# Performance work log

Hardware: AMD Instinct MI355X
Metric: run time of the kernel (lower is better)

## Reference

```python
import jax, jax.numpy as jnp
import numpy as np

REGION_NUM = 8  # DRConv2d default region_num


def setup_inputs() -> dict:
    key = jax.random.key(0)
    ks = jax.random.split(key, 10)
    B, H, W = 4, 256, 256
    C = 64   # n_fea_middle
    r = REGION_NUM
    s = 0.05
    return {
        "rgb":  jax.random.normal(ks[0], (B, 3, H, W), jnp.float32),
        "edge": jax.random.normal(ks[1], (B, 1, H, W), jnp.float32),
        # conv1: 1x1, 4 -> C
        "W1":  jax.random.normal(ks[2], (C, 4), jnp.float32) * s,
        "b1":  jax.random.normal(ks[3], (C,), jnp.float32) * s,
        # DRConv kernel-generator stage 1: Conv2d(C, r*r, 1)
        "Wk1": jax.random.normal(ks[4], (r * r, C), jnp.float32) * s,
        "bk1": jax.random.normal(ks[5], (r * r,), jnp.float32) * s,
        # stage 2: Conv2d(r*r, r*C*C, 1, groups=r) -> per group: r inputs, C*C outputs
        "Wk2": jax.random.normal(ks[6], (r, C * C, r), jnp.float32) * s,
        "bk2": jax.random.normal(ks[7], (r, C * C), jnp.float32) * s,
        # conv_guide: Conv2d(C, r, 1)
        "Wg":  jax.random.normal(ks[8], (r, C), jnp.float32) * s,
        "bg":  jax.random.normal(ks[9], (r,), jnp.float32) * s,
    }


def reference(rgb, edge, W1, b1, Wk1, bk1, Wk2, bk2, Wg, bg):
    r = REGION_NUM
    B = rgb.shape[0]
    # concat rgb+edge, 1x1 conv to n_fea_middle
    x = jnp.concatenate([rgb, edge], axis=1)                       # B,4,H,W
    x1 = jnp.einsum('bihw,oi->bohw', x, W1) + b1[None, :, None, None]  # B,C,H,W
    C = x1.shape[1]
    # ---- DRConv2d(C, C, kernel_size=1, region_num=r) ----
    # kernel-generating branch: AdaptiveAvgPool2d(1) == global mean for k=1
    g = jnp.mean(x1, axis=(2, 3))                                  # B,C
    t = jax.nn.sigmoid(g @ Wk1.T + bk1)                            # B,r*r
    tg = t.reshape(B, r, r)                                        # grouped 1x1 conv, groups=r
    k = jnp.einsum('bgi,goi->bgo', tg, Wk2) + bk2[None]            # B,r,C*C
    kernel = k.reshape(B, r, C, C)                                 # B,r,Cout,Cin
    # cross-correlation: per-batch, per-region 1x1 conv of x1 with generated kernel
    region_out = jnp.einsum('bchw,broc->brohw', x1, kernel)        # B,r,Cout,H,W
    # guide branch + hard region routing (asign_index forward)
    guide = jnp.einsum('bchw,rc->brhw', x1, Wg) + bg[None, :, None, None]  # B,r,H,W
    mask = jax.nn.one_hot(jnp.argmax(guide, axis=1), r, axis=1, dtype=x1.dtype)  # B,r,H,W
    out = jnp.sum(region_out * mask[:, :, None], axis=1)           # B,Cout,H,W
    return out
```

## Files before the change

kernel.cpp:

```cpp
#include <hip/hip_runtime.h>


#define HW_ 65536

__device__ double g_part[128];
__device__ double g_WgP[32];
__device__ double g_bgP[8];
__device__ __align__(16) float g_Wm[8192];
__device__ __align__(16) float g_Bm[2048];

typedef float f4v __attribute__((ext_vector_type(4)));

__global__ void k_sum(const float* __restrict__ rgb, const float* __restrict__ edge) {
    int plane = blockIdx.x;
    int chunk = blockIdx.y;
    int b = plane >> 2, ch = plane & 3;
    const float* src = (ch < 3) ? rgb + (size_t)(b * 3 + ch) * HW_
                                : edge + (size_t)b * HW_;
    src += chunk * 8192;
    int t = threadIdx.x;
    double s = 0.0;
    #pragma unroll
    for (int p = 0; p < 8; ++p) {
        float4 v = *(const float4*)(src + (p * 256 + t) * 4);
        s += (double)v.x + (double)v.y + (double)v.z + (double)v.w;
    }
    #pragma unroll
    for (int off = 32; off; off >>= 1) s += __shfl_down(s, off);
    __shared__ double wsum[4];
    if ((t & 63) == 0) wsum[t >> 6] = s;
    __syncthreads();
    if (t == 0) g_part[plane * 8 + chunk] = wsum[0] + wsum[1] + wsum[2] + wsum[3];
}

__global__ void k_params(const float* __restrict__ W1, const float* __restrict__ b1,
                         const float* __restrict__ Wk1, const float* __restrict__ bk1,
                         const float* __restrict__ Wk2, const float* __restrict__ bk2,
                         const float* __restrict__ Wg, const float* __restrict__ bg) {
    int blk = blockIdx.x;
    int b = blk >> 3, gr = blk & 7;
    int t = threadIdx.x;
    __shared__ double xm[16];
    __shared__ double gsh[64];
    __shared__ double tt_sh[8];
    __shared__ double red[4][64][5];

    if (t < 16) {
        double s = 0;
        #pragma unroll
        for (int i = 0; i < 8; ++i) s += g_part[t * 8 + i];
        xm[t] = s * (1.0 / 65536.0);
    }
    __syncthreads();
    if (t < 64) {
        double acc = (double)b1[t];
        #pragma unroll
        for (int j = 0; j < 4; ++j) acc += (double)W1[t * 4 + j] * xm[b * 4 + j];
        gsh[t] = acc;
    }
    __syncthreads();
    if (t < 8) {
        int j = gr * 8 + t;
        double z = (double)bk1[j];
        for (int c = 0; c < 64; ++c) z += (double)Wk1[j * 64 + c] * gsh[c];
        tt_sh[t] = 1.0 / (1.0 + exp(-z));
    }
    if (blk == 0) {
        if (t >= 64 && t < 96) {
            int r = (t - 64) >> 2, j = (t - 64) & 3;
            double a = 0;
            for (int c = 0; c < 64; ++c)
                a += (double)Wg[r * 64 + c] * (double)W1[c * 4 + j];
            g_WgP[t - 64] = a;
        } else if (t >= 96 && t < 104) {
            int r = t - 96;
            double a = (double)bg[r];
            for (int c = 0; c < 64; ++c)
                a += (double)Wg[r * 64 + c] * (double)b1[c];
            g_bgP[r] = a;
        }
    }
    __syncthreads();

    int o = t & 63, cq = t >> 6;
    double tt[8];
    #pragma unroll
    for (int i = 0; i < 8; ++i) tt[i] = tt_sh[i];
    double aw0 = 0, aw1 = 0, aw2 = 0, aw3 = 0, ab = 0;
    const float* wk2p = Wk2 + ((size_t)gr * 4096 + o * 64) * 8;
    const float* bk2p = bk2 + (size_t)gr * 4096 + o * 64;
    for (int c = cq * 16; c < cq * 16 + 16; ++c) {
        double ker = (double)bk2p[c];
        #pragma unroll
        for (int i = 0; i < 8; ++i)
            ker += tt[i] * (double)wk2p[c * 8 + i];
        aw0 += ker * (double)W1[c * 4 + 0];
        aw1 += ker * (double)W1[c * 4 + 1];
        aw2 += ker * (double)W1[c * 4 + 2];
        ab  += ker * (double)b1[c];
        aw3 += ker * (double)W1[c * 4 + 3];
    }
    red[cq][o][0] = aw0; red[cq][o][1] = aw1; red[cq][o][2] = aw2;
    red[cq][o][3] = aw3; red[cq][o][4] = ab;
    __syncthreads();
    if (t < 64) {
        double w0 = 0, w1 = 0, w2 = 0, w3 = 0, bb = 0;
        #pragma unroll
        for (int q = 0; q < 4; ++q) {
            w0 += red[q][t][0]; w1 += red[q][t][1]; w2 += red[q][t][2];
            w3 += red[q][t][3]; bb += red[q][t][4];
        }
        float* w = g_Wm + ((size_t)blk * 64 + t) * 4;
        w[0] = (float)w0; w[1] = (float)w1; w[2] = (float)w2; w[3] = (float)w3;
        g_Bm[blk * 64 + t] = (float)bb;
    }
}

__launch_bounds__(256)
__global__ void k_main(const float* __restrict__ rgb, const float* __restrict__ edge,
                       float* __restrict__ out) {
    __shared__ __align__(16) float sW[8 * 68];
    __shared__ __align__(16) float sB[8 * 20];
    __shared__ double sWg[32];
    __shared__ double sBg[8];
    int t = threadIdx.x;
    int b = blockIdx.y;
    int z = blockIdx.z;

    {
        if (t < 128) {
            int r = t >> 4, ol = t & 15;
            const float4* src = (const float4*)g_Wm;
            *(float4*)&sW[r * 68 + ol * 4] = src[(size_t)(b * 8 + r) * 64 + z * 16 + ol];
        } else {
            int idx = t - 128;
            int r = idx >> 4, ol = idx & 15;
            sB[r * 20 + ol] = g_Bm[(size_t)(b * 8 + r) * 64 + z * 16 + ol];
        }
        if (t < 32) sWg[t] = g_WgP[t];
        else if (t < 40) sBg[t - 32] = g_bgP[t - 32];
    }
    __syncthreads();

    float wg[32], bgf[8];
    #pragma unroll
    for (int i = 0; i < 32; ++i) wg[i] = (float)sWg[i];
    #pragma unroll
    for (int r = 0; r < 8; ++r) bgf[r] = (float)sBg[r];

    int pxb = (blockIdx.x * 256 + t) * 4;
    float xa[4], xb[4], xc[4], xd[4];
    {
        float4 v0 = *(const float4*)(rgb  + (size_t)(b * 3 + 0) * HW_ + pxb);
        float4 v1 = *(const float4*)(rgb  + (size_t)(b * 3 + 1) * HW_ + pxb);
        float4 v2 = *(const float4*)(rgb  + (size_t)(b * 3 + 2) * HW_ + pxb);
        float4 v3 = *(const float4*)(edge + (size_t)b * HW_ + pxb);
        xa[0] = v0.x; xa[1] = v0.y; xa[2] = v0.z; xa[3] = v0.w;
        xb[0] = v1.x; xb[1] = v1.y; xb[2] = v1.z; xb[3] = v1.w;
        xc[0] = v2.x; xc[1] = v2.y; xc[2] = v2.z; xc[3] = v2.w;
        xd[0] = v3.x; xd[1] = v3.y; xd[2] = v3.z; xd[3] = v3.w;
    }

    int reg[4];
    #pragma unroll
    for (int p = 0; p < 4; ++p) {
        float m1 = -1e30f, m2 = -1e30f; int bi = 0;
        #pragma unroll
        for (int r = 0; r < 8; ++r) {
            float gv = bgf[r] + wg[r * 4 + 0] * xa[p] + wg[r * 4 + 1] * xb[p]
                              + wg[r * 4 + 2] * xc[p] + wg[r * 4 + 3] * xd[p];
            if (gv > m1) { m2 = m1; m1 = gv; bi = r; }
            else if (gv > m2) { m2 = gv; }
        }
        if (m1 - m2 < 1e-4f) {
            double da = xa[p], db = xb[p], dc = xc[p], dd = xd[p];
            double bm = -1e300; bi = 0;
            #pragma unroll
            for (int r = 0; r < 8; ++r) {
                double gv = sBg[r] + sWg[r * 4 + 0] * da + sWg[r * 4 + 1] * db
                                   + sWg[r * 4 + 2] * dc + sWg[r * 4 + 3] * dd;
                if (gv > bm) { bm = gv; bi = r; }
            }
        }
        reg[p] = bi;
    }

    int base[4], bbase[4];
    #pragma unroll
    for (int p = 0; p < 4; ++p) { base[p] = reg[p] * 68; bbase[p] = reg[p] * 20; }

    float* outp = out + (size_t)(b * 64 + z * 16) * HW_ + pxb;
    #pragma unroll
    for (int oq = 0; oq < 4; ++oq) {
        float res[4][4];
        #pragma unroll
        for (int p = 0; p < 4; ++p) {
            float4 bq = *(const float4*)&sB[bbase[p] + oq * 4];
            float bqa[4] = {bq.x, bq.y, bq.z, bq.w};
            #pragma unroll
            for (int k = 0; k < 4; ++k) {
                float4 w = *(const float4*)&sW[base[p] + (oq * 4 + k) * 4];
                res[k][p] = bqa[k] + w.x * xa[p] + w.y * xb[p]
                                   + w.z * xc[p] + w.w * xd[p];
            }
        }
        #pragma unroll
        for (int k = 0; k < 4; ++k) {
            f4v pk; pk.x = res[k][0]; pk.y = res[k][1];
            pk.z = res[k][2]; pk.w = res[k][3];
            __builtin_nontemporal_store(pk, (f4v*)(outp + (size_t)(oq * 4 + k) * HW_));
        }
    }
}

extern "C" void kernel_launch(void* const* d_in, const int* in_sizes, int n_in,
                              void* d_out, int out_size, void* d_ws, size_t ws_size,
                              hipStream_t stream) {
    (void)d_ws; (void)ws_size;
    const float* rgb  = (const float*)d_in[0];
    const float* edge = (const float*)d_in[1];
    const float* W1   = (const float*)d_in[2];
    const float* b1   = (const float*)d_in[3];
    const float* Wk1  = (const float*)d_in[4];
    const float* bk1  = (const float*)d_in[5];
    const float* Wk2  = (const float*)d_in[6];
    const float* bk2  = (const float*)d_in[7];
    const float* Wg   = (const float*)d_in[8];
    const float* bg   = (const float*)d_in[9];
    float* out = (float*)d_out;

    k_sum<<<dim3(16, 8), 256, 0, stream>>>(rgb, edge);
    k_params<<<32, 256, 0, stream>>>(W1, b1, Wk1, bk1, Wk2, bk2, Wg, bg);
    k_main<<<dim3(64, 4, 4), 256, 0, stream>>>(rgb, edge, out);
}
```

Measured before the change: 113.0 us.

## Double grid parallelism, warp-parallelize param dot products, hoist input loads

```diff
diff --git a/kernel.cpp b/kernel.cpp
--- a/kernel.cpp
+++ b/kernel.cpp
@@ -3,13 +3,16 @@
 
 #define HW_ 65536
 
-__device__ double g_part[128];
+__device__ double g_part[256];
 __device__ double g_WgP[32];
 __device__ double g_bgP[8];
+__device__ float  g_WgPf[32];
+__device__ float  g_bgPf[8];
 __device__ __align__(16) float g_Wm[8192];
 __device__ __align__(16) float g_Bm[2048];
 
 typedef float f4v __attribute__((ext_vector_type(4)));
+typedef float f2v __attribute__((ext_vector_type(2)));
 
 __global__ void k_sum(const float* __restrict__ rgb, const float* __restrict__ edge) {
     int plane = blockIdx.x;
@@ -17,12 +20,12 @@
     int b = plane >> 2, ch = plane & 3;
     const float* src = (ch < 3) ? rgb + (size_t)(b * 3 + ch) * HW_
                                 : edge + (size_t)b * HW_;
-    src += chunk * 8192;
+    src += chunk * 4096;
     int t = threadIdx.x;
     double s = 0.0;
     #pragma unroll
-    for (int p = 0; p < 8; ++p) {
-        float4 v = *(const float4*)(src + (p * 256 + t) * 4);
+    for (int p = 0; p < 4; ++p) {
+        float4 v = ((const float4*)src)[p * 256 + t];
         s += (double)v.x + (double)v.y + (double)v.z + (double)v.w;
     }
     #pragma unroll
@@ -30,7 +33,7 @@
     __shared__ double wsum[4];
     if ((t & 63) == 0) wsum[t >> 6] = s;
     __syncthreads();
-    if (t == 0) g_part[plane * 8 + chunk] = wsum[0] + wsum[1] + wsum[2] + wsum[3];
+    if (t == 0) g_part[plane * 16 + chunk] = wsum[0] + wsum[1] + wsum[2] + wsum[3];
 }
 
 __global__ void k_params(const float* __restrict__ W1, const float* __restrict__ b1,
@@ -40,6 +43,7 @@
     int blk = blockIdx.x;
     int b = blk >> 3, gr = blk & 7;
     int t = threadIdx.x;
+    int w = t >> 6, l = t & 63;
     __shared__ double xm[16];
     __shared__ double gsh[64];
     __shared__ double tt_sh[8];
@@ -48,7 +52,7 @@
     if (t < 16) {
         double s = 0;
         #pragma unroll
-        for (int i = 0; i < 8; ++i) s += g_part[t * 8 + i];
+        for (int i = 0; i < 16; ++i) s += g_part[t * 16 + i];
         xm[t] = s * (1.0 / 65536.0);
     }
     __syncthreads();
@@ -59,25 +63,29 @@
         gsh[t] = acc;
     }
     __syncthreads();
-    if (t < 8) {
-        int j = gr * 8 + t;
-        double z = (double)bk1[j];
-        for (int c = 0; c < 64; ++c) z += (double)Wk1[j * 64 + c] * gsh[c];
-        tt_sh[t] = 1.0 / (1.0 + exp(-z));
+    #pragma unroll
+    for (int q = 0; q < 2; ++q) {
+        int jj = w * 2 + q;
+        int j = gr * 8 + jj;
+        double prod = (double)Wk1[j * 64 + l] * gsh[l];
+        #pragma unroll
+        for (int off = 32; off; off >>= 1) prod += __shfl_down(prod, off);
+        if (l == 0) tt_sh[jj] = 1.0 / (1.0 + exp(-(prod + (double)bk1[j])));
     }
     if (blk == 0) {
-        if (t >= 64 && t < 96) {
-            int r = (t - 64) >> 2, j = (t - 64) & 3;
-            double a = 0;
-            for (int c = 0; c < 64; ++c)
-                a += (double)Wg[r * 64 + c] * (double)W1[c * 4 + j];
-            g_WgP[t - 64] = a;
-        } else if (t >= 96 && t < 104) {
-            int r = t - 96;
-            double a = (double)bg[r];
-            for (int c = 0; c < 64; ++c)
-                a += (double)Wg[r * 64 + c] * (double)b1[c];
-            g_bgP[r] = a;
+        for (int d = w; d < 40; d += 4) {
+            double prod;
+            if (d < 32) prod = (double)Wg[(d >> 2) * 64 + l] * (double)W1[l * 4 + (d & 3)];
+            else        prod = (double)Wg[(d - 32) * 64 + l] * (double)b1[l];
+            #pragma unroll
+            for (int off = 32; off; off >>= 1) prod += __shfl_down(prod, off);
+            if (l == 0) {
+                if (d < 32) { g_WgP[d] = prod; g_WgPf[d] = (float)prod; }
+                else {
+                    double a = (double)bg[d - 32] + prod;
+                    g_bgP[d - 32] = a; g_bgPf[d - 32] = (float)a;
+                }
+            }
         }
     }
     __syncthreads();
@@ -110,13 +118,13 @@
             w0 += red[q][t][0]; w1 += red[q][t][1]; w2 += red[q][t][2];
             w3 += red[q][t][3]; bb += red[q][t][4];
         }
-        float* w = g_Wm + ((size_t)blk * 64 + t) * 4;
-        w[0] = (float)w0; w[1] = (float)w1; w[2] = (float)w2; w[3] = (float)w3;
+        float* wv = g_Wm + ((size_t)blk * 64 + t) * 4;
+        wv[0] = (float)w0; wv[1] = (float)w1; wv[2] = (float)w2; wv[3] = (float)w3;
         g_Bm[blk * 64 + t] = (float)bb;
     }
 }
 
-__launch_bounds__(256)
+__launch_bounds__(256, 6)
 __global__ void k_main(const float* __restrict__ rgb, const float* __restrict__ edge,
                        float* __restrict__ out) {
     __shared__ __align__(16) float sW[8 * 68];
@@ -127,11 +135,17 @@
     int b = blockIdx.y;
     int z = blockIdx.z;
 
+    int pxb = (blockIdx.x * 256 + t) * 2;
+    f2v v0 = *(const f2v*)(rgb  + (size_t)(b * 3 + 0) * HW_ + pxb);
+    f2v v1 = *(const f2v*)(rgb  + (size_t)(b * 3 + 1) * HW_ + pxb);
+    f2v v2 = *(const f2v*)(rgb  + (size_t)(b * 3 + 2) * HW_ + pxb);
+    f2v v3 = *(const f2v*)(edge + (size_t)b * HW_ + pxb);
+
     {
         if (t < 128) {
             int r = t >> 4, ol = t & 15;
-            const float4* src = (const float4*)g_Wm;
-            *(float4*)&sW[r * 68 + ol * 4] = src[(size_t)(b * 8 + r) * 64 + z * 16 + ol];
+            *(float4*)&sW[r * 68 + ol * 4] =
+                ((const float4*)g_Wm)[(size_t)(b * 8 + r) * 64 + z * 16 + ol];
         } else {
             int idx = t - 128;
             int r = idx >> 4, ol = idx & 15;
@@ -144,26 +158,21 @@
 
     float wg[32], bgf[8];
     #pragma unroll
-    for (int i = 0; i < 32; ++i) wg[i] = (float)sWg[i];
-    #pragma unroll
-    for (int r = 0; r < 8; ++r) bgf[r] = (float)sBg[r];
-
-    int pxb = (blockIdx.x * 256 + t) * 4;
-    float xa[4], xb[4], xc[4], xd[4];
-    {
-        float4 v0 = *(const float4*)(rgb  + (size_t)(b * 3 + 0) * HW_ + pxb);
-        float4 v1 = *(const float4*)(rgb  + (size_t)(b * 3 + 1) * HW_ + pxb);
-        float4 v2 = *(const float4*)(rgb  + (size_t)(b * 3 + 2) * HW_ + pxb);
-        float4 v3 = *(const float4*)(edge + (size_t)b * HW_ + pxb);
-        xa[0] = v0.x; xa[1] = v0.y; xa[2] = v0.z; xa[3] = v0.w;
-        xb[0] = v1.x; xb[1] = v1.y; xb[2] = v1.z; xb[3] = v1.w;
-        xc[0] = v2.x; xc[1] = v2.y; xc[2] = v2.z; xc[3] = v2.w;
-        xd[0] = v3.x; xd[1] = v3.y; xd[2] = v3.z; xd[3] = v3.w;
-    }
-
-    int reg[4];
-    #pragma unroll
-    for (int p = 0; p < 4; ++p) {
+    for (int i = 0; i < 32; ++i)
+        wg[i] = __int_as_float(__builtin_amdgcn_readfirstlane(__float_as_int(g_WgPf[i])));
+    #pragma unroll
+    for (int r = 0; r < 8; ++r)
+        bgf[r] = __int_as_float(__builtin_amdgcn_readfirstlane(__float_as_int(g_bgPf[r])));
+
+    float xa[2], xb[2], xc[2], xd[2];
+    xa[0] = v0.x; xa[1] = v0.y;
+    xb[0] = v1.x; xb[1] = v1.y;
+    xc[0] = v2.x; xc[1] = v2.y;
+    xd[0] = v3.x; xd[1] = v3.y;
+
+    int reg[2];
+    #pragma unroll
+    for (int p = 0; p < 2; ++p) {
         float m1 = -1e30f, m2 = -1e30f; int bi = 0;
         #pragma unroll
         for (int r = 0; r < 8; ++r) {
@@ -185,30 +194,29 @@
         reg[p] = bi;
     }
 
-    int base[4], bbase[4];
-    #pragma unroll
-    for (int p = 0; p < 4; ++p) { base[p] = reg[p] * 68; bbase[p] = reg[p] * 20; }
+    int base[2], bbase[2];
+    #pragma unroll
+    for (int p = 0; p < 2; ++p) { base[p] = reg[p] * 68; bbase[p] = reg[p] * 20; }
 
     float* outp = out + (size_t)(b * 64 + z * 16) * HW_ + pxb;
     #pragma unroll
     for (int oq = 0; oq < 4; ++oq) {
-        float res[4][4];
-        #pragma unroll
-        for (int p = 0; p < 4; ++p) {
+        float res[4][2];
+        #pragma unroll
+        for (int p = 0; p < 2; ++p) {
             float4 bq = *(const float4*)&sB[bbase[p] + oq * 4];
             float bqa[4] = {bq.x, bq.y, bq.z, bq.w};
             #pragma unroll
             for (int k = 0; k < 4; ++k) {
-                float4 w = *(const float4*)&sW[base[p] + (oq * 4 + k) * 4];
-                res[k][p] = bqa[k] + w.x * xa[p] + w.y * xb[p]
-                                   + w.z * xc[p] + w.w * xd[p];
+                float4 wv = *(const float4*)&sW[base[p] + (oq * 4 + k) * 4];
+                res[k][p] = bqa[k] + wv.x * xa[p] + wv.y * xb[p]
+                                   + wv.z * xc[p] + wv.w * xd[p];
             }
         }
         #pragma unroll
         for (int k = 0; k < 4; ++k) {
-            f4v pk; pk.x = res[k][0]; pk.y = res[k][1];
-            pk.z = res[k][2]; pk.w = res[k][3];
-            __builtin_nontemporal_store(pk, (f4v*)(outp + (size_t)(oq * 4 + k) * HW_));
+            f2v pk; pk.x = res[k][0]; pk.y = res[k][1];
+            __builtin_nontemporal_store(pk, (f2v*)(outp + (size_t)(oq * 4 + k) * HW_));
         }
     }
 }
@@ -229,7 +237,7 @@
     const float* bg   = (const float*)d_in[9];
     float* out = (float*)d_out;
 
-    k_sum<<<dim3(16, 8), 256, 0, stream>>>(rgb, edge);
+    k_sum<<<dim3(16, 16), 256, 0, stream>>>(rgb, edge);
     k_params<<<32, 256, 0, stream>>>(W1, b1, Wk1, bk1, Wk2, bk2, Wg, bg);
-    k_main<<<dim3(64, 4, 4), 256, 0, stream>>>(rgb, edge, out);
-}
+    k_main<<<dim3(128, 4, 4), 256, 0, stream>>>(rgb, edge, out);
+}
```

Result: slower. 115.3 us (+2.0%).
